# Kernel optimization log

Measured on AMD Instinct MI355X. Metric: run time of the kernel, lower is better.

The kernel has to match this reference:

```python
import jax, jax.numpy as jnp
import numpy as np

B, S, H = 32, 2048, 1024

def setup_inputs() -> dict:
    key = jax.random.key(0)
    ks = jax.random.split(key, 8)
    scale = 1.0 / np.sqrt(H)
    return {
        "query": jax.random.normal(ks[0], (B, H), jnp.float32),
        "keys": jax.random.normal(ks[1], (B, S, H), jnp.float32),
        "Wa_w": jax.random.uniform(ks[2], (H, H), jnp.float32, -scale, scale),
        "Wa_b": jax.random.uniform(ks[3], (H,), jnp.float32, -scale, scale),
        "Ua_w": jax.random.uniform(ks[4], (H, H), jnp.float32, -scale, scale),
        "Ua_b": jax.random.uniform(ks[5], (H,), jnp.float32, -scale, scale),
        "Va_w": jax.random.uniform(ks[6], (1, H), jnp.float32, -scale, scale),
        "Va_b": jax.random.uniform(ks[7], (1,), jnp.float32, -scale, scale),
    }

def reference(query, keys, Wa_w, Wa_b, Ua_w, Ua_b, Va_w, Va_b):
    # q_proj: [B, 1, H]; k_proj: [B, S, H]
    q_proj = (jnp.einsum('bh,oh->bo', query, Wa_w) + Wa_b)[:, None, :]
    k_proj = jnp.einsum('bsh,oh->bso', keys, Ua_w) + Ua_b
    # scores: [B, S] via Va(tanh(...)).squeeze
    scores = jnp.einsum('bsh,h->bs', jnp.tanh(q_proj + k_proj), Va_w[0]) + Va_b[0]
    weights = jax.nn.softmax(scores, axis=1)[:, None, :]  # [B, 1, S]
    context = jnp.einsum('bqs,bsh->bqh', weights, keys)   # [B, 1, H]
    return (context, weights)
```

## Files before the change

kernel.cpp:

```cpp
#include <hip/hip_runtime.h>
#include <hip/hip_bf16.h>


#define BB 32
#define SS 2048
#define HH 1024

typedef float  f32x4  __attribute__((ext_vector_type(4)));
typedef __bf16 bf16x4 __attribute__((ext_vector_type(4)));
typedef __bf16 bf16x8 __attribute__((ext_vector_type(8)));

__device__ inline __bf16 f2bf(float f) {
  unsigned u = __builtin_bit_cast(unsigned, f);
  u = (u + 0x7FFFu + ((u >> 16) & 1u)) >> 16;
  unsigned short s = (unsigned short)u;
  return __builtin_bit_cast(__bf16, s);
}

__device__ inline float tanh_fast(float x) {
  x = fminf(fmaxf(x, -15.f), 15.f);
  float e = __expf(2.f * x);
  return (e - 1.f) / (e + 1.f);
}

__device__ __forceinline__ void gload16(const __bf16* g, __bf16* l) {
  __builtin_amdgcn_global_load_lds(
      (const __attribute__((address_space(1))) void*)g,
      (__attribute__((address_space(3))) void*)l, 16, 0, 0);
}

__global__ void k_convert_keys(const float* __restrict__ src, __bf16* __restrict__ dst) {
  size_t i = ((size_t)blockIdx.x * 256 + threadIdx.x) * 8;
  f32x4 a = *(const f32x4*)(src + i);
  f32x4 b = *(const f32x4*)(src + i + 4);
  bf16x8 o;
  o[0] = f2bf(a[0]); o[1] = f2bf(a[1]); o[2] = f2bf(a[2]); o[3] = f2bf(a[3]);
  o[4] = f2bf(b[0]); o[5] = f2bf(b[1]); o[6] = f2bf(b[2]); o[7] = f2bf(b[3]);
  *(bf16x8*)(dst + i) = o;
}

__global__ void k_convert_ua(const float* __restrict__ src, __bf16* __restrict__ dst) {
  size_t i = (size_t)blockIdx.x * 256 + threadIdx.x;
  f32x4 v = ((const f32x4*)src)[i];
  bf16x4 o;
  o[0] = f2bf(v[0]); o[1] = f2bf(v[1]); o[2] = f2bf(v[2]); o[3] = f2bf(v[3]);
  *(bf16x4*)(dst + i * 4) = o;
}

__global__ void k_qproj(const float* __restrict__ q, const float* __restrict__ wa,
                        const float* __restrict__ wab, const float* __restrict__ uab,
                        float* __restrict__ qpc) {
  int tid = threadIdx.x;
  int gid = blockIdx.x * 32 + (tid >> 3);
  int lane8 = tid & 7;
  int b = gid >> 10, o = gid & 1023;
  const f32x4* qv = (const f32x4*)(q + (size_t)b * HH);
  const f32x4* wv = (const f32x4*)(wa + (size_t)o * HH);
  float s = 0.f;
#pragma unroll 4
  for (int kk = lane8; kk < HH / 4; kk += 8) {
    f32x4 a = qv[kk], w = wv[kk];
    s += a[0] * w[0] + a[1] * w[1] + a[2] * w[2] + a[3] * w[3];
  }
  s += __shfl_xor(s, 1); s += __shfl_xor(s, 2); s += __shfl_xor(s, 4);
  if (lane8 == 0) qpc[(size_t)b * HH + o] = s + wab[o] + uab[o];
}

__global__ void __launch_bounds__(256) k_scores2(
    const __bf16* __restrict__ keysb, const __bf16* __restrict__ ua,
    const float* __restrict__ qpc, const float* __restrict__ vaw,
    float* __restrict__ spart) {
  __shared__ __align__(16) __bf16 Alds[128 * 32];
  __shared__ __align__(16) __bf16 Blds[128 * 32];
  __shared__ float scorebuf[128];

  int raw = blockIdx.x;
  int o = (raw >> 3) & 7;
  int m = ((raw >> 6) << 3) | (raw & 7);
  int b = m >> 4;
  long grow0 = (long)m * 128;
  int o0 = o * 128;

  int tid = threadIdx.x;
  int w = tid >> 6, lane = tid & 63;
  int wm = w >> 1, wn = w & 1;
  int ln = lane & 15, hi = lane >> 4;

  int lrow = lane >> 2;
  int lk = (lane & 3) * 8;
  const __bf16* ag0 = keysb + (size_t)(grow0 + w * 16 + lrow) * HH + lk;
  const __bf16* ag1 = ag0 + (size_t)64 * HH;
  const __bf16* bg0 = ua + (size_t)(o0 + w * 16 + lrow) * HH + lk;
  const __bf16* bg1 = bg0 + (size_t)64 * HH;
  __bf16* al0 = Alds + (w * 16) * 32;
  __bf16* al1 = Alds + (64 + w * 16) * 32;
  __bf16* bl0 = Blds + (w * 16) * 32;
  __bf16* bl1 = Blds + (64 + w * 16) * 32;

  f32x4 acc[4][4] = {};

  for (int kt = 0; kt < 32; ++kt) {
    if (kt) __syncthreads();
    gload16(ag0, al0); gload16(ag1, al1);
    gload16(bg0, bl0); gload16(bg1, bl1);
    ag0 += 32; ag1 += 32; bg0 += 32; bg1 += 32;
    __syncthreads();
    bf16x8 af[4], bfr[4];
#pragma unroll
    for (int mi = 0; mi < 4; ++mi)
      af[mi] = *(const bf16x8*)(Alds + (wm * 64 + mi * 16 + ln) * 32 + hi * 8);
#pragma unroll
    for (int ni = 0; ni < 4; ++ni)
      bfr[ni] = *(const bf16x8*)(Blds + (wn * 64 + ni * 16 + ln) * 32 + hi * 8);
#pragma unroll
    for (int mi = 0; mi < 4; ++mi)
#pragma unroll
      for (int ni = 0; ni < 4; ++ni)
        acc[mi][ni] = __builtin_amdgcn_mfma_f32_16x16x32_bf16(af[mi], bfr[ni], acc[mi][ni], 0, 0, 0);
  }

  float qv[4], vv[4];
#pragma unroll
  for (int ni = 0; ni < 4; ++ni) {
    int oc = o0 + wn * 64 + ni * 16 + ln;
    qv[ni] = qpc[(size_t)b * HH + oc];
    vv[ni] = vaw[oc];
  }
  float rsum[4][4];
#pragma unroll
  for (int mi = 0; mi < 4; ++mi)
#pragma unroll
    for (int j = 0; j < 4; ++j) {
      float v = 0.f;
#pragma unroll
      for (int ni = 0; ni < 4; ++ni)
        v += tanh_fast(acc[mi][ni][j] + qv[ni]) * vv[ni];
      v += __shfl_xor(v, 1); v += __shfl_xor(v, 2);
      v += __shfl_xor(v, 4); v += __shfl_xor(v, 8);
      rsum[mi][j] = v;
    }
  if (wn == 1 && ln == 0) {
#pragma unroll
    for (int mi = 0; mi < 4; ++mi)
#pragma unroll
      for (int j = 0; j < 4; ++j)
        scorebuf[wm * 64 + mi * 16 + hi * 4 + j] = rsum[mi][j];
  }
  __syncthreads();
  if (wn == 0 && ln == 0) {
#pragma unroll
    for (int mi = 0; mi < 4; ++mi)
#pragma unroll
      for (int j = 0; j < 4; ++j) {
        int rl = wm * 64 + mi * 16 + hi * 4 + j;
        spart[(size_t)o * (BB * SS) + grow0 + rl] = rsum[mi][j] + scorebuf[rl];
      }
  }
}

__global__ void __launch_bounds__(256) k_scores_fused(
    const float* __restrict__ keys, const __bf16* __restrict__ ua,
    const float* __restrict__ qpc, const float* __restrict__ vaw,
    float* __restrict__ spart) {
  __shared__ __bf16 Alds[128][40];
  __shared__ float scorebuf[128];

  int raw = blockIdx.x;
  int o = (raw >> 3) & 7;
  int m = ((raw >> 6) << 3) | (raw & 7);
  int b = m >> 4;
  long grow0 = (long)m * 128;
  int o0 = o * 128;

  int tid = threadIdx.x;
  int w = tid >> 6, lane = tid & 63;
  int wm = w >> 1, wn = w & 1;
  int ln = lane & 15, hi = lane >> 4;

  int srow = tid >> 3;
  int sk4 = tid & 7;
  const f32x4* keysv = (const f32x4*)keys;
  const bf16x8* uav = (const bf16x8*)ua;

  f32x4 acc[4][4] = {};

  for (int kt = 0; kt < 32; ++kt) {
    int k0 = kt * 32;
    bf16x8 bf[4];
#pragma unroll
    for (int ni = 0; ni < 4; ++ni) {
      int oc = o0 + wn * 64 + ni * 16 + ln;
      bf[ni] = uav[(size_t)oc * (HH / 8) + (k0 >> 3) + hi];
    }
    f32x4 st[4];
#pragma unroll
    for (int p = 0; p < 4; ++p)
      st[p] = keysv[((size_t)(grow0 + srow + 32 * p) << 8) + (size_t)(kt * 8 + sk4)];
    __syncthreads();
#pragma unroll
    for (int p = 0; p < 4; ++p) {
      bf16x4 t;
      t[0] = f2bf(st[p][0]); t[1] = f2bf(st[p][1]);
      t[2] = f2bf(st[p][2]); t[3] = f2bf(st[p][3]);
      *(bf16x4*)&Alds[srow + 32 * p][sk4 * 4] = t;
    }
    __syncthreads();
    bf16x8 af[4];
#pragma unroll
    for (int mi = 0; mi < 4; ++mi)
      af[mi] = *(const bf16x8*)&Alds[wm * 64 + mi * 16 + ln][hi * 8];
#pragma unroll
    for (int mi = 0; mi < 4; ++mi)
#pragma unroll
      for (int ni = 0; ni < 4; ++ni)
        acc[mi][ni] = __builtin_amdgcn_mfma_f32_16x16x32_bf16(af[mi], bf[ni], acc[mi][ni], 0, 0, 0);
  }

  float qv[4], vv[4];
#pragma unroll
  for (int ni = 0; ni < 4; ++ni) {
    int oc = o0 + wn * 64 + ni * 16 + ln;
    qv[ni] = qpc[(size_t)b * HH + oc];
    vv[ni] = vaw[oc];
  }
  float rsum[4][4];
#pragma unroll
  for (int mi = 0; mi < 4; ++mi)
#pragma unroll
    for (int j = 0; j < 4; ++j) {
      float v = 0.f;
#pragma unroll
      for (int ni = 0; ni < 4; ++ni)
        v += tanh_fast(acc[mi][ni][j] + qv[ni]) * vv[ni];
      v += __shfl_xor(v, 1); v += __shfl_xor(v, 2);
      v += __shfl_xor(v, 4); v += __shfl_xor(v, 8);
      rsum[mi][j] = v;
    }
  if (wn == 1 && ln == 0) {
#pragma unroll
    for (int mi = 0; mi < 4; ++mi)
#pragma unroll
      for (int j = 0; j < 4; ++j)
        scorebuf[wm * 64 + mi * 16 + hi * 4 + j] = rsum[mi][j];
  }
  __syncthreads();
  if (wn == 0 && ln == 0) {
#pragma unroll
    for (int mi = 0; mi < 4; ++mi)
#pragma unroll
      for (int j = 0; j < 4; ++j) {
        int rl = wm * 64 + mi * 16 + hi * 4 + j;
        spart[(size_t)o * (BB * SS) + grow0 + rl] = rsum[mi][j] + scorebuf[rl];
      }
  }
}

__global__ void k_softmax(const float* __restrict__ spart, float* __restrict__ wout) {
  int b = blockIdx.x, tid = threadIdx.x;
  __shared__ float red[8];
  int w = tid >> 6;
  float sc[8];
  float mx = -1e30f;
#pragma unroll
  for (int i = 0; i < 8; ++i) {
    int s = tid + i * 256;
    float v = 0.f;
#pragma unroll
    for (int ot = 0; ot < 8; ++ot) v += spart[(size_t)ot * (BB * SS) + b * SS + s];
    sc[i] = v; mx = fmaxf(mx, v);
  }
#pragma unroll
  for (int off = 1; off < 64; off <<= 1) mx = fmaxf(mx, __shfl_xor(mx, off));
  if ((tid & 63) == 0) red[w] = mx;
  __syncthreads();
  mx = fmaxf(fmaxf(red[0], red[1]), fmaxf(red[2], red[3]));
  float sum = 0.f;
#pragma unroll
  for (int i = 0; i < 8; ++i) { sc[i] = __expf(sc[i] - mx); sum += sc[i]; }
#pragma unroll
  for (int off = 1; off < 64; off <<= 1) sum += __shfl_xor(sum, off);
  if ((tid & 63) == 0) red[4 + w] = sum;
  __syncthreads();
  sum = (red[4] + red[5]) + (red[6] + red[7]);
  float inv = 1.f / sum;
#pragma unroll
  for (int i = 0; i < 8; ++i) wout[(size_t)b * SS + tid + i * 256] = sc[i] * inv;
}

__global__ void k_ctx_part(const float* __restrict__ keys, const float* __restrict__ wts,
                           float* __restrict__ cpart) {
  int bc = blockIdx.x;
  int b = bc >> 4, sc = bc & 15;
  int tid = threadIdx.x;
  int s0 = sc * 128;
  const f32x4* kv = (const f32x4*)keys;
  f32x4 a0 = {0,0,0,0}, a1 = {0,0,0,0}, a2 = {0,0,0,0}, a3 = {0,0,0,0};
  for (int s = 0; s < 128; s += 4) {
    size_t base = (size_t)b * SS + s0 + s;
    a0 += wts[base + 0] * kv[(base + 0) * (HH / 4) + tid];
    a1 += wts[base + 1] * kv[(base + 1) * (HH / 4) + tid];
    a2 += wts[base + 2] * kv[(base + 2) * (HH / 4) + tid];
    a3 += wts[base + 3] * kv[(base + 3) * (HH / 4) + tid];
  }
  f32x4 a = (a0 + a1) + (a2 + a3);
  ((f32x4*)cpart)[(size_t)bc * (HH / 4) + tid] = a;
}

__global__ void k_ctx_red(const float* __restrict__ cpart, float* __restrict__ ctx) {
  int i = blockIdx.x * 256 + threadIdx.x;
  int b = i >> 10, h = i & 1023;
  float v = 0.f;
#pragma unroll
  for (int sc = 0; sc < 16; ++sc) v += cpart[((size_t)(b * 16 + sc)) * HH + h];
  ctx[i] = v;
}

extern "C" void kernel_launch(void* const* d_in, const int* in_sizes, int n_in,
                              void* d_out, int out_size, void* d_ws, size_t ws_size,
                              hipStream_t stream) {
  (void)in_sizes; (void)n_in; (void)out_size;
  const float* query = (const float*)d_in[0];
  const float* keys  = (const float*)d_in[1];
  const float* wa_w  = (const float*)d_in[2];
  const float* wa_b  = (const float*)d_in[3];
  const float* ua_w  = (const float*)d_in[4];
  const float* ua_b  = (const float*)d_in[5];
  const float* va_w  = (const float*)d_in[6];

  char* ws = (char*)d_ws;
  float* ctx_out = (float*)d_out;
  float* w_out   = ctx_out + BB * HH;

  const size_t need = (size_t)135 << 20;
  if (ws_size >= need) {
    __bf16* keys_bf = (__bf16*)ws;
    __bf16* ua_bf   = (__bf16*)(ws + ((size_t)128 << 20));
    float*  qpc     = (float*)(ws + ((size_t)130 << 20));
    float*  spart   = (float*)(ws + ((size_t)131 << 20));
    float*  cpart   = (float*)(ws + ((size_t)133 << 20));

    k_qproj<<<1024, 256, 0, stream>>>(query, wa_w, wa_b, ua_b, qpc);
    k_convert_ua<<<1024, 256, 0, stream>>>(ua_w, ua_bf);
    k_convert_keys<<<BB * SS * HH / (256 * 8), 256, 0, stream>>>(keys, keys_bf);
    k_scores2<<<4096, 256, 0, stream>>>(keys_bf, ua_bf, qpc, va_w, spart);
    k_softmax<<<BB, 256, 0, stream>>>(spart, w_out);
    k_ctx_part<<<512, 256, 0, stream>>>(keys, w_out, cpart);
    k_ctx_red<<<BB * HH / 256, 256, 0, stream>>>(cpart, ctx_out);
  } else {
    __bf16* ua_bf  = (__bf16*)ws;
    float*  qpc    = (float*)(ws + (2u << 20));
    float*  spart  = (float*)(ws + (2u << 20) + (128u << 10));
    float*  cpart  = (float*)(ws + (4u << 20) + (128u << 10));

    k_convert_ua<<<1024, 256, 0, stream>>>(ua_w, ua_bf);
    k_qproj<<<1024, 256, 0, stream>>>(query, wa_w, wa_b, ua_b, qpc);
    k_scores_fused<<<4096, 256, 0, stream>>>(keys, ua_bf, qpc, va_w, spart);
    k_softmax<<<BB, 256, 0, stream>>>(spart, w_out);
    k_ctx_part<<<512, 256, 0, stream>>>(keys, w_out, cpart);
    k_ctx_red<<<BB * HH / 256, 256, 0, stream>>>(cpart, ctx_out);
  }
}
```

Baseline: 310.3 us.

## Triple-buffer key tiles, read Ua from global, use bf16 keys for context

Rewrites the score GEMM main loop. Key tiles are loaded through a three-stage LDS ring buffer with prefetch two steps ahead and a single barrier per iteration, and a swizzled layout is used to reduce LDS bank conflicts. The Ua operand is now read directly from global memory into registers instead of going through LDS, and MFMA issue runs at raised priority. The context kernel now reads the bf16 copy of keys instead of the fp32 original, which halves its memory traffic but lowers the precision of the context output.

```diff
diff --git a/kernel.cpp b/kernel.cpp
--- a/kernel.cpp
+++ b/kernel.cpp
@@ -5,6 +5,7 @@
 #define BB 32
 #define SS 2048
 #define HH 1024
+#define TSZ (128 * 32)
 
 typedef float  f32x4  __attribute__((ext_vector_type(4)));
 typedef __bf16 bf16x4 __attribute__((ext_vector_type(4)));
@@ -15,6 +16,12 @@
   u = (u + 0x7FFFu + ((u >> 16) & 1u)) >> 16;
   unsigned short s = (unsigned short)u;
   return __builtin_bit_cast(__bf16, s);
+}
+
+__device__ inline float bf2f(__bf16 b) {
+  unsigned short s = __builtin_bit_cast(unsigned short, b);
+  unsigned u = ((unsigned)s) << 16;
+  return __builtin_bit_cast(float, u);
 }
 
 __device__ inline float tanh_fast(float x) {
@@ -66,12 +73,11 @@
   if (lane8 == 0) qpc[(size_t)b * HH + o] = s + wab[o] + uab[o];
 }
 
-__global__ void __launch_bounds__(256) k_scores2(
+__global__ void __launch_bounds__(256) k_scores3(
     const __bf16* __restrict__ keysb, const __bf16* __restrict__ ua,
     const float* __restrict__ qpc, const float* __restrict__ vaw,
     float* __restrict__ spart) {
-  __shared__ __align__(16) __bf16 Alds[128 * 32];
-  __shared__ __align__(16) __bf16 Blds[128 * 32];
+  __shared__ __align__(16) __bf16 Alds[3 * TSZ];
   __shared__ float scorebuf[128];
 
   int raw = blockIdx.x;
@@ -87,36 +93,61 @@
   int ln = lane & 15, hi = lane >> 4;
 
   int lrow = lane >> 2;
-  int lk = (lane & 3) * 8;
-  const __bf16* ag0 = keysb + (size_t)(grow0 + w * 16 + lrow) * HH + lk;
-  const __bf16* ag1 = ag0 + (size_t)64 * HH;
-  const __bf16* bg0 = ua + (size_t)(o0 + w * 16 + lrow) * HH + lk;
-  const __bf16* bg1 = bg0 + (size_t)64 * HH;
-  __bf16* al0 = Alds + (w * 16) * 32;
-  __bf16* al1 = Alds + (64 + w * 16) * 32;
-  __bf16* bl0 = Blds + (w * 16) * 32;
-  __bf16* bl1 = Blds + (64 + w * 16) * 32;
+  int sig = ((lane & 3) - ((lane >> 3) & 3)) & 3;
+  const __bf16* agA = keysb + (size_t)(grow0 + w * 16 + lrow) * HH + sig * 8;
+  const __bf16* agB = agA + (size_t)64 * HH;
+  int ldsA = (w * 16) * 32;
+  int ldsB = (64 + w * 16) * 32;
+
+  const __bf16* bp0 = ua + (size_t)(o0 + wn * 64 + 0 * 16 + ln) * HH + hi * 8;
+  const __bf16* bp1 = ua + (size_t)(o0 + wn * 64 + 1 * 16 + ln) * HH + hi * 8;
+  const __bf16* bp2 = ua + (size_t)(o0 + wn * 64 + 2 * 16 + ln) * HH + hi * 8;
+  const __bf16* bp3 = ua + (size_t)(o0 + wn * 64 + 3 * 16 + ln) * HH + hi * 8;
+
+  int slot_a = (hi + ((ln >> 1) & 3)) & 3;
+  int arow0 = (wm * 64 + ln) * 32 + slot_a * 8;
 
   f32x4 acc[4][4] = {};
 
+  gload16(agA, Alds + 0 * TSZ + ldsA);
+  gload16(agB, Alds + 0 * TSZ + ldsB);
+  gload16(agA + 32, Alds + 1 * TSZ + ldsA);
+  gload16(agB + 32, Alds + 1 * TSZ + ldsB);
+  asm volatile("s_waitcnt vmcnt(2)" ::: "memory");
+  __builtin_amdgcn_sched_barrier(0);
+
+  int rdoff = 0;
   for (int kt = 0; kt < 32; ++kt) {
-    if (kt) __syncthreads();
-    gload16(ag0, al0); gload16(ag1, al1);
-    gload16(bg0, bl0); gload16(bg1, bl1);
-    ag0 += 32; ag1 += 32; bg0 += 32; bg1 += 32;
-    __syncthreads();
-    bf16x8 af[4], bfr[4];
-#pragma unroll
-    for (int mi = 0; mi < 4; ++mi)
-      af[mi] = *(const bf16x8*)(Alds + (wm * 64 + mi * 16 + ln) * 32 + hi * 8);
-#pragma unroll
-    for (int ni = 0; ni < 4; ++ni)
-      bfr[ni] = *(const bf16x8*)(Blds + (wn * 64 + ni * 16 + ln) * 32 + hi * 8);
+    __builtin_amdgcn_s_barrier();
+    __builtin_amdgcn_sched_barrier(0);
+
+    bf16x8 bfr[4];
+    bfr[0] = *(const bf16x8*)bp0; bp0 += 32;
+    bfr[1] = *(const bf16x8*)bp1; bp1 += 32;
+    bfr[2] = *(const bf16x8*)bp2; bp2 += 32;
+    bfr[3] = *(const bf16x8*)bp3; bp3 += 32;
+
+    int kn = (kt + 2 <= 31) ? kt + 2 : 31;
+    int wroff = rdoff + 2 * TSZ; if (wroff >= 3 * TSZ) wroff -= 3 * TSZ;
+    gload16(agA + kn * 32, Alds + wroff + ldsA);
+    gload16(agB + kn * 32, Alds + wroff + ldsB);
+
+    bf16x8 af[4];
+#pragma unroll
+    for (int mi = 0; mi < 4; ++mi)
+      af[mi] = *(const bf16x8*)(Alds + rdoff + arow0 + mi * 16 * 32);
+
+    __builtin_amdgcn_s_setprio(1);
 #pragma unroll
     for (int mi = 0; mi < 4; ++mi)
 #pragma unroll
       for (int ni = 0; ni < 4; ++ni)
-        acc[mi][ni] = __builtin_amdgcn_mfma_f32_16x16x32_bf16(af[mi], bfr[ni], acc[mi][ni], 0, 0, 0);
+        acc[mi][ni] = __builtin_amdgcn_mfma_f32_16x16x32_bf16(
+            af[mi], (ni == 0 ? bfr[0] : ni == 1 ? bfr[1] : ni == 2 ? bfr[2] : bfr[3]),
+            acc[mi][ni], 0, 0, 0);
+    __builtin_amdgcn_s_setprio(0);
+
+    rdoff += TSZ; if (rdoff == 3 * TSZ) rdoff = 0;
   }
 
   float qv[4], vv[4];
@@ -285,6 +316,32 @@
   float inv = 1.f / sum;
 #pragma unroll
   for (int i = 0; i < 8; ++i) wout[(size_t)b * SS + tid + i * 256] = sc[i] * inv;
+}
+
+__global__ void k_ctx_part_bf(const __bf16* __restrict__ keysb, const float* __restrict__ wts,
+                              float* __restrict__ cpart) {
+  int bc = blockIdx.x;
+  int b = bc >> 4, sc = bc & 15;
+  int tid = threadIdx.x;
+  int s0 = sc * 128;
+  f32x4 a0 = {0,0,0,0}, a1 = {0,0,0,0}, a2 = {0,0,0,0}, a3 = {0,0,0,0};
+  for (int s = 0; s < 128; s += 4) {
+    size_t base = (size_t)b * SS + s0 + s;
+    float w0 = wts[base + 0], w1 = wts[base + 1], w2 = wts[base + 2], w3 = wts[base + 3];
+    bf16x4 k0 = *(const bf16x4*)(keysb + (base + 0) * HH + tid * 4);
+    bf16x4 k1 = *(const bf16x4*)(keysb + (base + 1) * HH + tid * 4);
+    bf16x4 k2 = *(const bf16x4*)(keysb + (base + 2) * HH + tid * 4);
+    bf16x4 k3 = *(const bf16x4*)(keysb + (base + 3) * HH + tid * 4);
+#pragma unroll
+    for (int j = 0; j < 4; ++j) {
+      a0[j] += w0 * bf2f(k0[j]);
+      a1[j] += w1 * bf2f(k1[j]);
+      a2[j] += w2 * bf2f(k2[j]);
+      a3[j] += w3 * bf2f(k3[j]);
+    }
+  }
+  f32x4 a = (a0 + a1) + (a2 + a3);
+  ((f32x4*)cpart)[(size_t)bc * (HH / 4) + tid] = a;
 }
 
 __global__ void k_ctx_part(const float* __restrict__ keys, const float* __restrict__ wts,
@@ -342,9 +399,9 @@
     k_qproj<<<1024, 256, 0, stream>>>(query, wa_w, wa_b, ua_b, qpc);
     k_convert_ua<<<1024, 256, 0, stream>>>(ua_w, ua_bf);
     k_convert_keys<<<BB * SS * HH / (256 * 8), 256, 0, stream>>>(keys, keys_bf);
-    k_scores2<<<4096, 256, 0, stream>>>(keys_bf, ua_bf, qpc, va_w, spart);
+    k_scores3<<<4096, 256, 0, stream>>>(keys_bf, ua_bf, qpc, va_w, spart);
     k_softmax<<<BB, 256, 0, stream>>>(spart, w_out);
-    k_ctx_part<<<512, 256, 0, stream>>>(keys, w_out, cpart);
+    k_ctx_part_bf<<<512, 256, 0, stream>>>(keys_bf, w_out, cpart);
     k_ctx_red<<<BB * HH / 256, 256, 0, stream>>>(cpart, ctx_out);
   } else {
     __bf16* ua_bf  = (__bf16*)ws;
```

Measured after the change: 377.1 us. +21.5%, slower.
